# Performance work log

Hardware: AMD Instinct MI355X
Metric: run time of the kernel (lower is better)

Reference implementation:

```python
import jax, jax.numpy as jnp
import numpy as np

DIM = 2048
NUM_HEADS = 16
HEAD_DIM = DIM // NUM_HEADS  # 128
LATENT = 512
THETA = 10000.0


def rotate_half(x):
    # interleaved rotate: (x0,x1,x2,x3,...) -> (-x1,x0,-x3,x2,...)
    x1 = x[..., ::2]
    x2 = x[..., 1::2]
    return jnp.stack((-x2, x1), axis=-1).reshape(x.shape)


def apply_rope(x, sin, cos):
    return x * cos + rotate_half(x) * sin


def setup_inputs() -> dict:
    key = jax.random.key(0)
    ks = jax.random.split(key, 6)
    s_in = 1.0 / np.sqrt(DIM)
    s_lat = 1.0 / np.sqrt(LATENT)
    x = jax.random.normal(ks[0], (2, 2048, DIM), dtype=jnp.float32)
    Wq = jax.random.normal(ks[1], (DIM, DIM), dtype=jnp.float32) * s_in
    Wdkv = jax.random.normal(ks[2], (DIM, 2 * LATENT), dtype=jnp.float32) * s_in
    Wuk = jax.random.normal(ks[3], (LATENT, DIM), dtype=jnp.float32) * s_lat
    Wuv = jax.random.normal(ks[4], (LATENT, DIM), dtype=jnp.float32) * s_lat
    Wo = jax.random.normal(ks[5], (DIM, DIM), dtype=jnp.float32) * s_in
    return {"x": x, "Wq": Wq, "Wdkv": Wdkv, "Wuk": Wuk, "Wuv": Wuv, "Wo": Wo}


def reference(x, Wq, Wdkv, Wuk, Wuv, Wo):
    b, s, _ = x.shape
    # q projection -> [b, h, s, hd]
    q = (x @ Wq).reshape(b, s, NUM_HEADS, HEAD_DIM).transpose(0, 2, 1, 3)
    # low-rank latent down-projection, then up-project K and V
    dkv = x @ Wdkv  # [b, s, 2*L]
    dk, dv = dkv[..., :LATENT], dkv[..., LATENT:]
    k = (dk @ Wuk).reshape(b, s, NUM_HEADS, HEAD_DIM).transpose(0, 2, 1, 3)
    v = (dv @ Wuv).reshape(b, s, NUM_HEADS, HEAD_DIM).transpose(0, 2, 1, 3)
    # RoPE cache (concatenated freqs, matching the torch module)
    inv_freq = 1.0 / (THETA ** (jnp.arange(0, HEAD_DIM, 2, dtype=jnp.float32) / HEAD_DIM))
    t = jnp.arange(s, dtype=jnp.float32)
    freqs = t[:, None] * inv_freq[None, :]          # [s, hd/2]
    emb = jnp.concatenate([freqs, freqs], axis=-1)  # [s, hd]
    sin, cos = jnp.sin(emb), jnp.cos(emb)
    q = apply_rope(q, sin, cos)
    k = apply_rope(k, sin, cos)
    # SDPA (no mask, no dropout): scale = 1/sqrt(head_dim)
    scores = jnp.einsum('bhqd,bhkd->bhqk', q, k) / jnp.sqrt(jnp.float32(HEAD_DIM))
    attn = jax.nn.softmax(scores, axis=-1)
    out = jnp.einsum('bhqk,bhkd->bhqd', attn, v)
    out = out.transpose(0, 2, 1, 3).reshape(b, s, DIM)
    return out @ Wo
```

## Files before the change

kernel.cpp:

```cpp
#include <hip/hip_runtime.h>
#include <hip/hip_bf16.h>
#include <stdint.h>

typedef __attribute__((ext_vector_type(8))) __bf16 bf16x8;
typedef __attribute__((ext_vector_type(4))) float f32x4;

__device__ __forceinline__ unsigned short f2bf(float f) {
  union { float f; unsigned u; } v; v.f = f;
  unsigned r = v.u + 0x7FFFu + ((v.u >> 16) & 1u);
  return (unsigned short)(r >> 16);
}

__device__ __forceinline__ float fast_exp2(float x) {
#if __has_builtin(__builtin_amdgcn_exp2f)
  return __builtin_amdgcn_exp2f(x);
#else
  return exp2f(x);
#endif
}

__device__ __forceinline__ void gload_lds16(const void* g, void* l) {
  __builtin_amdgcn_global_load_lds((const __attribute__((address_space(1))) void*)g,
                                   (__attribute__((address_space(3))) void*)l,
                                   16, 0, 0);
}


__global__ void k_rope(float* __restrict__ cosT, float* __restrict__ sinT) {
  int idx = blockIdx.x * blockDim.x + threadIdx.x;
  int t = idx >> 6, j = idx & 63;
  float inv = powf(10000.f, -(float)j / 64.f);
  float ang = (float)t * inv;
  cosT[idx] = cosf(ang);
  sinT[idx] = sinf(ang);
}

__global__ void k_cvt_bf16(const float* __restrict__ in, unsigned short* __restrict__ out, int n) {
  int i = (blockIdx.x * blockDim.x + threadIdx.x) * 4;
  if (i >= n) return;
  float4 v = *reinterpret_cast<const float4*>(in + i);
  ushort4 o;
  o.x = f2bf(v.x); o.y = f2bf(v.y); o.z = f2bf(v.z); o.w = f2bf(v.w);
  *reinterpret_cast<ushort4*>(out + i) = o;
}

__global__ __launch_bounds__(256) void k_transpose_cvt(const float* __restrict__ in,
                                                       unsigned short* __restrict__ out,
                                                       int K, int N) {
  __shared__ float t[32][33];
  int nt = blockIdx.x, kt = blockIdx.y;
  int tx = threadIdx.x, ty = threadIdx.y;
#pragma unroll
  for (int i = 0; i < 4; i++)
    t[ty + i * 8][tx] = in[(size_t)(kt * 32 + ty + i * 8) * N + nt * 32 + tx];
  __syncthreads();
#pragma unroll
  for (int i = 0; i < 4; i++)
    out[(size_t)(nt * 32 + ty + i * 8) * K + kt * 32 + tx] = f2bf(t[tx][ty + i * 8]);
}

template <int EPI>
__global__ __launch_bounds__(256, 2) void k_gemm(
    const unsigned short* __restrict__ A, int lda,
    const unsigned short* __restrict__ BT, int ldb,
    void* __restrict__ Cout, void* __restrict__ Cout2, int M, int N, int K,
    const float* __restrict__ cosT, const float* __restrict__ sinT) {
  __shared__ __attribute__((aligned(16))) unsigned short As[128 * 64];
  __shared__ __attribute__((aligned(16))) unsigned short Bs[128 * 64];
  const int tid = threadIdx.x;
  const int lane = tid & 63;
  const int w = tid >> 6;
  const int wr = w >> 1, wc = w & 1;
  const int m0 = blockIdx.y * 128, n0 = blockIdx.x * 128;

  f32x4 acc[4][4] = {};

  const int srow = w * 8 + (lane >> 3);
  const int sch = (lane & 7) * 8;
  const unsigned short* gA = A + (size_t)(m0 + srow) * lda + sch;
  const unsigned short* gB = BT + (size_t)(n0 + srow) * ldb + sch;
  unsigned short* lA = &As[srow * 64 + sch];
  unsigned short* lB = &Bs[srow * 64 + sch];

  for (int kt = 0; kt < K; kt += 64) {
    __syncthreads();
#pragma unroll
    for (int i = 0; i < 4; i++) {
      gload_lds16(gA + (size_t)(i * 32) * lda + kt, lA + i * 32 * 64);
      gload_lds16(gB + (size_t)(i * 32) * ldb + kt, lB + i * 32 * 64);
    }
    __syncthreads();
#pragma unroll
    for (int kk = 0; kk < 64; kk += 32) {
      bf16x8 af[4], bfr[4];
#pragma unroll
      for (int m = 0; m < 4; m++)
        af[m] = *reinterpret_cast<const bf16x8*>(&As[(wr * 64 + m * 16 + (lane & 15)) * 64 + kk + (lane >> 4) * 8]);
#pragma unroll
      for (int n = 0; n < 4; n++)
        bfr[n] = *reinterpret_cast<const bf16x8*>(&Bs[(wc * 64 + n * 16 + (lane & 15)) * 64 + kk + (lane >> 4) * 8]);
#pragma unroll
      for (int m = 0; m < 4; m++)
#pragma unroll
        for (int n = 0; n < 4; n++) {
          if (EPI == 3)
            acc[m][n] = __builtin_amdgcn_mfma_f32_16x16x32_bf16(bfr[n], af[m], acc[m][n], 0, 0, 0);
          else
            acc[m][n] = __builtin_amdgcn_mfma_f32_16x16x32_bf16(af[m], bfr[n], acc[m][n], 0, 0, 0);
        }
    }
  }

  const int rl = (lane >> 4) * 4;
  const int cl = lane & 15;
#pragma unroll
  for (int m = 0; m < 4; m++)
#pragma unroll
    for (int n = 0; n < 4; n++)
#pragma unroll
      for (int r = 0; r < 4; r++) {
        float v = acc[m][n][r];
        if (EPI == 4) {
          int gr = m0 + wr * 64 + m * 16 + rl + r;
          int gc = n0 + wc * 64 + n * 16 + cl;
          ((float*)Cout)[(size_t)gr * N + gc] = v;
        } else if (EPI == 1) {
          int gr = m0 + wr * 64 + m * 16 + rl + r;
          int gc = n0 + wc * 64 + n * 16 + cl;
          int b = gr >> 11, s = gr & 2047, h = gc >> 7, d = gc & 127;
          float p = __shfl_xor(v, 1);
          float c = cosT[s * 64 + (d & 63)];
          float sn = sinT[s * 64 + (d & 63)];
          v = v * c + ((d & 1) ? p : -p) * sn;
          ((unsigned short*)Cout)[((size_t)(b * 16 + h) * 2048 + s) * 128 + d] = f2bf(v);
        } else if (EPI == 5) {
          int gr = m0 + wr * 64 + m * 16 + rl + r;
          int gc = n0 + wc * 64 + n * 16 + cl;
          if (n0 < 2048) {
            int b = gr >> 11, s = gr & 2047, h = gc >> 7, d = gc & 127;
            float p = __shfl_xor(v, 1);
            float c = cosT[s * 64 + (d & 63)];
            float sn = sinT[s * 64 + (d & 63)];
            v = v * c + ((d & 1) ? p : -p) * sn;
            ((unsigned short*)Cout)[((size_t)(b * 16 + h) * 2048 + s) * 128 + d] = f2bf(v);
          } else {
            ((unsigned short*)Cout2)[(size_t)gr * 1024 + (gc - 2048)] = f2bf(v);
          }
        } else {
          int gd = n0 + wc * 64 + n * 16 + rl + r;
          int gs = m0 + wr * 64 + m * 16 + cl;
          int b = gs >> 11, s = gs & 2047, h = gd >> 7, d = gd & 127;
          ((unsigned short*)Cout)[((size_t)(b * 16 + h) * 128 + d) * 2048 + s] = f2bf(v);
        }
      }
}

__global__ __launch_bounds__(256, 2) void k_attn(
    const unsigned short* __restrict__ Q,
    const unsigned short* __restrict__ Kt,
    const unsigned short* __restrict__ Vt,
    unsigned short* __restrict__ O) {
  __shared__ __attribute__((aligned(16))) unsigned short Kls[2][64 * 128];
  __shared__ __attribute__((aligned(16))) unsigned short Vls[2][128 * 64];
  __shared__ __attribute__((aligned(16))) unsigned short Pls[128 * 64];
  const int flat = blockIdx.x + (blockIdx.y << 4);
  const int swz = (flat & 7) * 64 + (flat >> 3);
  const int qt = swz & 15, bh = swz >> 4;
  const int tid = threadIdx.x, lane = tid & 63, w = tid >> 6;
  const unsigned short* Qh = Q + (size_t)bh * 2048 * 128;
  const unsigned short* Kh = Kt + (size_t)bh * 2048 * 128;
  const unsigned short* Vh = Vt + (size_t)bh * 128 * 2048;
  const int q0 = qt * 128;

  bf16x8 qf[2][4];
#pragma unroll
  for (int m = 0; m < 2; m++)
#pragma unroll
    for (int kd = 0; kd < 4; kd++) {
      int row = q0 + w * 32 + m * 16 + (lane & 15);
      int k = kd * 32 + (lane >> 4) * 8;
      qf[m][kd] = *reinterpret_cast<const bf16x8*>(Qh + (size_t)row * 128 + k);
    }

  f32x4 accO[2][8] = {};
  float lsum[2] = {0.f, 0.f};

  const int kr0 = w * 4 + (lane >> 4);
  const int kcb = lane & 15;
  const int vr0 = w * 8 + (lane >> 3);
  const int vcb = lane & 7;

  auto stage = [&](int buf, int kt) {
#pragma unroll
    for (int i = 0; i < 4; i++) {
      int rr = kr0 + i * 16;
      gload_lds16(Kh + (size_t)(kt * 64 + rr) * 128 + ((kcb ^ (rr & 7)) * 8),
                  (char*)Kls + buf * 16384 + rr * 256 + kcb * 16);
    }
#pragma unroll
    for (int i = 0; i < 4; i++) {
      int rr = vr0 + i * 32;
      gload_lds16(Vh + (size_t)rr * 2048 + kt * 64 + ((vcb ^ (rr & 7)) * 8),
                  (char*)Vls + buf * 16384 + rr * 128 + vcb * 16);
    }
  };

  stage(0, 0);
  __syncthreads();

  const float CL2 = 0.08838834764831845f * 1.44269504088896f;

  for (int kt = 0; kt < 32; kt++) {
    const int cur = kt & 1;
    if (kt + 1 < 32) stage(cur ^ 1, kt + 1);

    f32x4 accT[4][2] = {};
#pragma unroll
    for (int kd = 0; kd < 4; kd++) {
      bf16x8 kf[4];
#pragma unroll
      for (int n = 0; n < 4; n++) {
        int row = n * 16 + (lane & 15);
        int byte = cur * 16384 + row * 256 + (((kd * 32 + (lane >> 4) * 8) * 2) ^ ((row & 7) << 4));
        kf[n] = *reinterpret_cast<const bf16x8*>((const char*)Kls + byte);
      }
      __builtin_amdgcn_s_setprio(1);
#pragma unroll
      for (int n = 0; n < 4; n++)
#pragma unroll
        for (int m = 0; m < 2; m++)
          accT[n][m] = __builtin_amdgcn_mfma_f32_16x16x32_bf16(kf[n], qf[m][kd], accT[n][m], 0, 0, 0);
      __builtin_amdgcn_s_setprio(0);
    }

#pragma unroll
    for (int n = 0; n < 4; n++)
#pragma unroll
      for (int m = 0; m < 2; m++) {
        float p0 = fast_exp2(accT[n][m][0] * CL2);
        float p1 = fast_exp2(accT[n][m][1] * CL2);
        float p2 = fast_exp2(accT[n][m][2] * CL2);
        float p3 = fast_exp2(accT[n][m][3] * CL2);
        lsum[m] += (p0 + p1) + (p2 + p3);
        unsigned pk0, pk1;
        asm("v_cvt_pk_bf16_f32 %0, %1, %2" : "=v"(pk0) : "v"(p0), "v"(p1));
        asm("v_cvt_pk_bf16_f32 %0, %1, %2" : "=v"(pk1) : "v"(p2), "v"(p3));
        int row = w * 32 + m * 16 + (lane & 15);
        int kcol = n * 16 + (lane >> 4) * 4;
        int byte = row * 128 + ((kcol * 2) ^ ((row & 7) << 4));
        uint2 pk = {pk0, pk1};
        *reinterpret_cast<uint2*>((char*)Pls + byte) = pk;
      }

#pragma unroll
    for (int kk = 0; kk < 2; kk++) {
      bf16x8 pf[2], vf[8];
#pragma unroll
      for (int m = 0; m < 2; m++) {
        int row = w * 32 + m * 16 + (lane & 15);
        int byte = row * 128 + (((kk * 32 + (lane >> 4) * 8) * 2) ^ ((row & 7) << 4));
        pf[m] = *reinterpret_cast<const bf16x8*>((const char*)Pls + byte);
      }
#pragma unroll
      for (int n = 0; n < 8; n++) {
        int row = n * 16 + (lane & 15);
        int byte = cur * 16384 + row * 128 + (((kk * 32 + (lane >> 4) * 8) * 2) ^ ((row & 7) << 4));
        vf[n] = *reinterpret_cast<const bf16x8*>((const char*)Vls + byte);
      }
      __builtin_amdgcn_s_setprio(1);
#pragma unroll
      for (int m = 0; m < 2; m++)
#pragma unroll
        for (int n = 0; n < 8; n++)
          accO[m][n] = __builtin_amdgcn_mfma_f32_16x16x32_bf16(pf[m], vf[n], accO[m][n], 0, 0, 0);
      __builtin_amdgcn_s_setprio(0);
    }

    __syncthreads();
  }

  const int rl = (lane >> 4) * 4;
  float rv[2][4];
#pragma unroll
  for (int m = 0; m < 2; m++) {
    float s = lsum[m];
    s += __shfl_xor(s, 16);
    s += __shfl_xor(s, 32);
    float inv = 1.0f / s;
#pragma unroll
    for (int r = 0; r < 4; r++) rv[m][r] = __shfl(inv, rl + r);
  }

  const int b = bh >> 4, h = bh & 15;
#pragma unroll
  for (int m = 0; m < 2; m++)
#pragma unroll
    for (int n = 0; n < 8; n++)
#pragma unroll
      for (int r = 0; r < 4; r++) {
        int s = q0 + w * 32 + m * 16 + rl + r;
        int d = n * 16 + (lane & 15);
        O[((size_t)(b * 2048 + s)) * 2048 + h * 128 + d] = f2bf(accO[m][n][r] * rv[m][r]);
      }
}


extern "C" void kernel_launch(void* const* d_in, const int* in_sizes, int n_in,
                              void* d_out, int out_size, void* d_ws, size_t ws_size,
                              hipStream_t stream) {
  const float* x    = (const float*)d_in[0];
  const float* Wq   = (const float*)d_in[1];
  const float* Wdkv = (const float*)d_in[2];
  const float* Wuk  = (const float*)d_in[3];
  const float* Wuv  = (const float*)d_in[4];
  const float* Wo   = (const float*)d_in[5];

  char* ws = (char*)d_ws;
  unsigned short* xb    = (unsigned short*)(ws + 0);
  unsigned short* WqT   = (unsigned short*)(ws + 16777216);
  unsigned short* WdkvT = (unsigned short*)(ws + 25165824);
  unsigned short* WukT  = (unsigned short*)(ws + 29360128);
  unsigned short* WuvT  = (unsigned short*)(ws + 31457280);
  unsigned short* dkv   = (unsigned short*)(ws + 33554432);
  unsigned short* q_att = (unsigned short*)(ws + 41943040);
  unsigned short* k_att = (unsigned short*)(ws + 58720256);
  unsigned short* vT    = (unsigned short*)(ws + 75497472);
  float* cosT           = (float*)(ws + 92274688);
  float* sinT           = (float*)(ws + 92798976);

  k_rope<<<512, 256, 0, stream>>>(cosT, sinT);
  k_cvt_bf16<<<8192, 256, 0, stream>>>(x, xb, 2 * 2048 * 2048);
  k_transpose_cvt<<<dim3(64, 64), dim3(32, 8), 0, stream>>>(Wq, WqT, 2048, 2048);
  k_transpose_cvt<<<dim3(32, 64), dim3(32, 8), 0, stream>>>(Wdkv, WdkvT, 2048, 1024);
  k_transpose_cvt<<<dim3(64, 16), dim3(32, 8), 0, stream>>>(Wuk, WukT, 512, 2048);
  k_transpose_cvt<<<dim3(64, 16), dim3(32, 8), 0, stream>>>(Wuv, WuvT, 512, 2048);

  k_gemm<5><<<dim3(24, 32), 256, 0, stream>>>(xb, 2048, WqT, 2048, q_att, dkv, 4096, 3072, 2048, cosT, sinT);
  k_transpose_cvt<<<dim3(64, 64), dim3(32, 8), 0, stream>>>(Wo, WqT, 2048, 2048);
  k_gemm<1><<<dim3(16, 32), 256, 0, stream>>>(dkv, 1024, WukT, 512, k_att, nullptr, 4096, 2048, 512, cosT, sinT);
  k_gemm<3><<<dim3(16, 32), 256, 0, stream>>>(dkv + 512, 1024, WuvT, 512, vT, nullptr, 4096, 2048, 512, nullptr, nullptr);
  k_attn<<<dim3(16, 32), 256, 0, stream>>>(q_att, k_att, vT, xb);
  k_gemm<4><<<dim3(16, 32), 256, 0, stream>>>(xb, 2048, WqT, 2048, (float*)d_out, nullptr, 4096, 2048, 2048, nullptr, nullptr);
}
```

Before: 261.6 us.

## Fuse K/V up-projection GEMMs and load V fragments directly from global in attention

The separate K and V up-projection GEMMs become one launch (EPI 6). It treats the contiguous WukT/WuvT buffers as one 4096-wide B matrix, picks the A column offset and the MFMA operand order per block, and writes RoPE'd K or transposed V. In the attention kernel, V is no longer staged through LDS. Each wave reads its V MFMA fragments straight from global memory into registers, and launch bounds rise to 3 blocks per CU to use the freed LDS. The cost is that all four waves fetch the same V tile from global/L2 with no LDS sharing, and the global-load latency sits inside the loop.

```diff
diff --git a/kernel.cpp b/kernel.cpp
--- a/kernel.cpp
+++ b/kernel.cpp
@@ -72,12 +72,14 @@
   const int w = tid >> 6;
   const int wr = w >> 1, wc = w & 1;
   const int m0 = blockIdx.y * 128, n0 = blockIdx.x * 128;
+  const bool swp = (EPI == 3) || (EPI == 6 && n0 >= 2048);
 
   f32x4 acc[4][4] = {};
 
   const int srow = w * 8 + (lane >> 3);
   const int sch = (lane & 7) * 8;
-  const unsigned short* gA = A + (size_t)(m0 + srow) * lda + sch;
+  const unsigned short* Aeff = (EPI == 6 && n0 >= 2048) ? A + 512 : A;
+  const unsigned short* gA = Aeff + (size_t)(m0 + srow) * lda + sch;
   const unsigned short* gB = BT + (size_t)(n0 + srow) * ldb + sch;
   unsigned short* lA = &As[srow * 64 + sch];
   unsigned short* lB = &Bs[srow * 64 + sch];
@@ -99,15 +101,19 @@
 #pragma unroll
       for (int n = 0; n < 4; n++)
         bfr[n] = *reinterpret_cast<const bf16x8*>(&Bs[(wc * 64 + n * 16 + (lane & 15)) * 64 + kk + (lane >> 4) * 8]);
-#pragma unroll
-      for (int m = 0; m < 4; m++)
-#pragma unroll
-        for (int n = 0; n < 4; n++) {
-          if (EPI == 3)
+      if (swp) {
+#pragma unroll
+        for (int m = 0; m < 4; m++)
+#pragma unroll
+          for (int n = 0; n < 4; n++)
             acc[m][n] = __builtin_amdgcn_mfma_f32_16x16x32_bf16(bfr[n], af[m], acc[m][n], 0, 0, 0);
-          else
+      } else {
+#pragma unroll
+        for (int m = 0; m < 4; m++)
+#pragma unroll
+          for (int n = 0; n < 4; n++)
             acc[m][n] = __builtin_amdgcn_mfma_f32_16x16x32_bf16(af[m], bfr[n], acc[m][n], 0, 0, 0);
-        }
+      }
     }
   }
 
@@ -146,6 +152,22 @@
           } else {
             ((unsigned short*)Cout2)[(size_t)gr * 1024 + (gc - 2048)] = f2bf(v);
           }
+        } else if (EPI == 6) {
+          if (n0 < 2048) {
+            int gr = m0 + wr * 64 + m * 16 + rl + r;
+            int gc = n0 + wc * 64 + n * 16 + cl;
+            int b = gr >> 11, s = gr & 2047, h = gc >> 7, d = gc & 127;
+            float p = __shfl_xor(v, 1);
+            float c = cosT[s * 64 + (d & 63)];
+            float sn = sinT[s * 64 + (d & 63)];
+            v = v * c + ((d & 1) ? p : -p) * sn;
+            ((unsigned short*)Cout)[((size_t)(b * 16 + h) * 2048 + s) * 128 + d] = f2bf(v);
+          } else {
+            int gd = (n0 - 2048) + wc * 64 + n * 16 + rl + r;
+            int gs = m0 + wr * 64 + m * 16 + cl;
+            int b = gs >> 11, s = gs & 2047, h = gd >> 7, d = gd & 127;
+            ((unsigned short*)Cout2)[((size_t)(b * 16 + h) * 128 + d) * 2048 + s] = f2bf(v);
+          }
         } else {
           int gd = n0 + wc * 64 + n * 16 + rl + r;
           int gs = m0 + wr * 64 + m * 16 + cl;
@@ -155,13 +177,12 @@
       }
 }
 
-__global__ __launch_bounds__(256, 2) void k_attn(
+__global__ __launch_bounds__(256, 3) void k_attn(
     const unsigned short* __restrict__ Q,
     const unsigned short* __restrict__ Kt,
     const unsigned short* __restrict__ Vt,
     unsigned short* __restrict__ O) {
   __shared__ __attribute__((aligned(16))) unsigned short Kls[2][64 * 128];
-  __shared__ __attribute__((aligned(16))) unsigned short Vls[2][128 * 64];
   __shared__ __attribute__((aligned(16))) unsigned short Pls[128 * 64];
   const int flat = blockIdx.x + (blockIdx.y << 4);
   const int swz = (flat & 7) * 64 + (flat >> 3);
@@ -187,32 +208,30 @@
 
   const int kr0 = w * 4 + (lane >> 4);
   const int kcb = lane & 15;
-  const int vr0 = w * 8 + (lane >> 3);
-  const int vcb = lane & 7;
-
-  auto stage = [&](int buf, int kt) {
+  const unsigned short* Vbase = Vh + (size_t)(lane & 15) * 2048 + (lane >> 4) * 8;
+
+  auto stageK = [&](int buf, int kt) {
 #pragma unroll
     for (int i = 0; i < 4; i++) {
       int rr = kr0 + i * 16;
       gload_lds16(Kh + (size_t)(kt * 64 + rr) * 128 + ((kcb ^ (rr & 7)) * 8),
                   (char*)Kls + buf * 16384 + rr * 256 + kcb * 16);
     }
-#pragma unroll
-    for (int i = 0; i < 4; i++) {
-      int rr = vr0 + i * 32;
-      gload_lds16(Vh + (size_t)rr * 2048 + kt * 64 + ((vcb ^ (rr & 7)) * 8),
-                  (char*)Vls + buf * 16384 + rr * 128 + vcb * 16);
-    }
   };
 
-  stage(0, 0);
+  stageK(0, 0);
   __syncthreads();
 
   const float CL2 = 0.08838834764831845f * 1.44269504088896f;
 
   for (int kt = 0; kt < 32; kt++) {
     const int cur = kt & 1;
-    if (kt + 1 < 32) stage(cur ^ 1, kt + 1);
+    if (kt + 1 < 32) stageK(cur ^ 1, kt + 1);
+
+    bf16x8 vf0[8];
+#pragma unroll
+    for (int n = 0; n < 8; n++)
+      vf0[n] = *reinterpret_cast<const bf16x8*>(Vbase + (size_t)(n * 16) * 2048 + kt * 64);
 
     f32x4 accT[4][2] = {};
 #pragma unroll
@@ -252,29 +271,39 @@
         *reinterpret_cast<uint2*>((char*)Pls + byte) = pk;
       }
 
-#pragma unroll
-    for (int kk = 0; kk < 2; kk++) {
-      bf16x8 pf[2], vf[8];
-#pragma unroll
-      for (int m = 0; m < 2; m++) {
-        int row = w * 32 + m * 16 + (lane & 15);
-        int byte = row * 128 + (((kk * 32 + (lane >> 4) * 8) * 2) ^ ((row & 7) << 4));
-        pf[m] = *reinterpret_cast<const bf16x8*>((const char*)Pls + byte);
-      }
-#pragma unroll
-      for (int n = 0; n < 8; n++) {
-        int row = n * 16 + (lane & 15);
-        int byte = cur * 16384 + row * 128 + (((kk * 32 + (lane >> 4) * 8) * 2) ^ ((row & 7) << 4));
-        vf[n] = *reinterpret_cast<const bf16x8*>((const char*)Vls + byte);
-      }
-      __builtin_amdgcn_s_setprio(1);
-#pragma unroll
-      for (int m = 0; m < 2; m++)
-#pragma unroll
-        for (int n = 0; n < 8; n++)
-          accO[m][n] = __builtin_amdgcn_mfma_f32_16x16x32_bf16(pf[m], vf[n], accO[m][n], 0, 0, 0);
-      __builtin_amdgcn_s_setprio(0);
-    }
+    bf16x8 pfA[2];
+#pragma unroll
+    for (int m = 0; m < 2; m++) {
+      int row = w * 32 + m * 16 + (lane & 15);
+      int byte = row * 128 + ((((lane >> 4) * 8) * 2) ^ ((row & 7) << 4));
+      pfA[m] = *reinterpret_cast<const bf16x8*>((const char*)Pls + byte);
+    }
+    bf16x8 vf1[8];
+#pragma unroll
+    for (int n = 0; n < 8; n++)
+      vf1[n] = *reinterpret_cast<const bf16x8*>(Vbase + (size_t)(n * 16) * 2048 + kt * 64 + 32);
+    __builtin_amdgcn_s_setprio(1);
+#pragma unroll
+    for (int m = 0; m < 2; m++)
+#pragma unroll
+      for (int n = 0; n < 8; n++)
+        accO[m][n] = __builtin_amdgcn_mfma_f32_16x16x32_bf16(pfA[m], vf0[n], accO[m][n], 0, 0, 0);
+    __builtin_amdgcn_s_setprio(0);
+
+    bf16x8 pfB[2];
+#pragma unroll
+    for (int m = 0; m < 2; m++) {
+      int row = w * 32 + m * 16 + (lane & 15);
+      int byte = row * 128 + (((32 + (lane >> 4) * 8) * 2) ^ ((row & 7) << 4));
+      pfB[m] = *reinterpret_cast<const bf16x8*>((const char*)Pls + byte);
+    }
+    __builtin_amdgcn_s_setprio(1);
+#pragma unroll
+    for (int m = 0; m < 2; m++)
+#pragma unroll
+      for (int n = 0; n < 8; n++)
+        accO[m][n] = __builtin_amdgcn_mfma_f32_16x16x32_bf16(pfB[m], vf1[n], accO[m][n], 0, 0, 0);
+    __builtin_amdgcn_s_setprio(0);
 
     __syncthreads();
   }
@@ -337,8 +366,7 @@
 
   k_gemm<5><<<dim3(24, 32), 256, 0, stream>>>(xb, 2048, WqT, 2048, q_att, dkv, 4096, 3072, 2048, cosT, sinT);
   k_transpose_cvt<<<dim3(64, 64), dim3(32, 8), 0, stream>>>(Wo, WqT, 2048, 2048);
-  k_gemm<1><<<dim3(16, 32), 256, 0, stream>>>(dkv, 1024, WukT, 512, k_att, nullptr, 4096, 2048, 512, cosT, sinT);
-  k_gemm<3><<<dim3(16, 32), 256, 0, stream>>>(dkv + 512, 1024, WuvT, 512, vT, nullptr, 4096, 2048, 512, nullptr, nullptr);
+  k_gemm<6><<<dim3(32, 32), 256, 0, stream>>>(dkv, 1024, WukT, 512, k_att, vT, 4096, 4096, 512, cosT, sinT);
   k_attn<<<dim3(16, 32), 256, 0, stream>>>(q_att, k_att, vT, xb);
   k_gemm<4><<<dim3(16, 32), 256, 0, stream>>>(xb, 2048, WqT, 2048, (float*)d_out, nullptr, 4096, 2048, 2048, nullptr, nullptr);
 }
```

New measurement: 636.6 us. 143% more time.
